# Kernel optimization log

Measured on AMD Instinct MI355X. Metric: run time of the kernel, lower is better.

## Reference

```python
import jax, jax.numpy as jnp
import numpy as np
from jax import lax

K, N = 256, 65536

def setup_inputs() -> dict:
    key = jax.random.key(0)
    k1, k2, k3 = jax.random.split(key, 3)
    # obs: non-negative event counts [K, N]
    obs = jax.random.uniform(k1, (K, N), dtype=jnp.float32) * 4.0
    # Beta ~ U(1, 3) [K]
    Beta = 1.0 + 2.0 * jax.random.uniform(k2, (K,), dtype=jnp.float32)
    # Alpha ~ U(0, 0.01) [K, K]
    Alpha = 0.01 * jax.random.uniform(k3, (K, K), dtype=jnp.float32)
    return {"obs": obs, "Beta": Beta, "Alpha": Alpha}

def reference(obs, Beta, Alpha):
    # obs: [K, N], Beta: [K], Alpha: [K, K]
    Kk, Nn = obs.shape
    Mu0 = obs.mean(axis=1) / 10.0 + 0.01            # [K] background rate
    decay = jnp.exp(-Beta)                          # [K]

    # Exponential kernel sum S[t] = sum_{tp<t} obs[:,tp] * Beta * exp(-(t-tp)*Beta)
    # admits recursion H[t] = exp(-Beta) * (H[t-1] + obs[:, t-1]), S[t] = Beta * H[t]
    def step(h, o_prev):
        h_new = decay * (h + o_prev)
        return h_new, h_new

    _, H = lax.scan(step, jnp.zeros((Kk,), obs.dtype), obs[:, :Nn - 1].T)  # [N-1, K]
    S = H * Beta                                    # [N-1, K]
    # lam1[:, t] = softplus(Alpha @ S[t]) for t >= 1; lam1[:, 0] = 0 (by original code)
    lam = jax.nn.softplus(jnp.einsum('jk,tk->tj', Alpha, S))  # [N-1, K]
    lams1 = jnp.concatenate([jnp.zeros((Kk, 1), obs.dtype), lam.T], axis=1)  # [K, N]
    lams0 = jnp.broadcast_to(Mu0[:, None], (Kk, Nn))          # [K, N]

    Nloglams = obs * jnp.log(lams0 + lams1 + 1e-5)
    loglik = (Nloglams - lams0 - lams1).sum()
    return loglik, lams0, lams1
```

## Files before the change

### kernel.cpp

```cpp
#include <hip/hip_runtime.h>
#include <math.h>

#define KK 256
#define NN 65536
#define TT 128
#define WW 16
#define TPAD 264
#define NB (NN / TT)
#define NCHUNK (NB * 2)

typedef __bf16 bf16x8 __attribute__((ext_vector_type(8)));
typedef float f32x4 __attribute__((ext_vector_type(4)));

__global__ __launch_bounds__(256) void alpha_kernel(const float* __restrict__ Alpha,
                                                    __bf16* __restrict__ AlphaB,
                                                    float* __restrict__ out) {
  const int i = blockIdx.x * 256 + threadIdx.x;
  AlphaB[i] = (__bf16)Alpha[i];
  if (i == 0) out[0] = 0.f;
}

__global__ __launch_bounds__(512, 4) void main_kernel(const float* __restrict__ obs,
                                                      const float* __restrict__ Beta,
                                                      const __bf16* __restrict__ AlphaB,
                                                      float* __restrict__ out,
                                                      float* __restrict__ P) {
  __shared__ __bf16 Slds[TT][TPAD];
  const int tid = threadIdx.x;
  const int bid = blockIdx.x;
  const int tb = ((bid & 7) << 6) | (bid >> 3);
  const int t0 = tb * TT;

  {
    const int k = tid & 255;
    const int c = tid >> 8;
    const int tbase = t0 + (c << 6);
    const float beta = Beta[k];
    const float decay = expf(-beta);
    const float* row = obs + (size_t)k * NN;
    float g = 0.f;
    if (tbase > 0) {
      const float4* p = (const float4*)(row + tbase - WW);
#pragma unroll
      for (int i = 0; i < WW / 4; ++i) {
        float4 v = p[i];
        g = decay * (g + v.x);
        g = decay * (g + v.y);
        g = decay * (g + v.z);
        g = decay * (g + v.w);
      }
    }
    const int r0 = c << 6;
    Slds[r0][k] = (__bf16)(beta * g);
    const float4* q = (const float4*)(row + tbase);
    float s = 0.f;
#pragma unroll
    for (int i = 0; i < 15; ++i) {
      float4 v = q[i];
      s += (v.x + v.y) + (v.z + v.w);
      g = decay * (g + v.x); Slds[r0 + 4 * i + 1][k] = (__bf16)(beta * g);
      g = decay * (g + v.y); Slds[r0 + 4 * i + 2][k] = (__bf16)(beta * g);
      g = decay * (g + v.z); Slds[r0 + 4 * i + 3][k] = (__bf16)(beta * g);
      g = decay * (g + v.w); Slds[r0 + 4 * i + 4][k] = (__bf16)(beta * g);
    }
    {
      float4 v = q[15];
      s += (v.x + v.y) + (v.z + v.w);
      g = decay * (g + v.x); Slds[r0 + 61][k] = (__bf16)(beta * g);
      g = decay * (g + v.y); Slds[r0 + 62][k] = (__bf16)(beta * g);
      g = decay * (g + v.z); Slds[r0 + 63][k] = (__bf16)(beta * g);
    }
    P[(size_t)(2 * bid + c) * KK + k] = s;
  }
  __syncthreads();

  const int wave = tid >> 6;
  const int wj = wave & 3, wc = wave >> 2;
  const int lane = tid & 63;
  const int lquad = lane >> 4;
  const int l16 = lane & 15;

  f32x4 acc[4][4];
#pragma unroll
  for (int a = 0; a < 4; ++a)
#pragma unroll
    for (int b = 0; b < 4; ++b) acc[a][b] = (f32x4){0.f, 0.f, 0.f, 0.f};

  const __bf16* Abase = AlphaB + (size_t)(wj * 64 + l16) * KK + lquad * 8;
  for (int k0 = 0; k0 < KK; k0 += 32) {
    bf16x8 afrag[4], bfrag[4];
#pragma unroll
    for (int js = 0; js < 4; ++js)
      afrag[js] = *(const bf16x8*)(Abase + (size_t)js * 16 * KK + k0);
#pragma unroll
    for (int ts = 0; ts < 4; ++ts)
      bfrag[ts] = *(const bf16x8*)&Slds[wc * 64 + ts * 16 + l16][k0 + lquad * 8];
#pragma unroll
    for (int js = 0; js < 4; ++js)
#pragma unroll
      for (int ts = 0; ts < 4; ++ts)
        acc[js][ts] = __builtin_amdgcn_mfma_f32_16x16x32_bf16(
            afrag[js], bfrag[ts], acc[js][ts], 0, 0, 0);
  }

  float* lams1 = out + 1 + (size_t)KK * NN;
  const int tcol = t0 + wc * 64;
#pragma unroll
  for (int js = 0; js < 4; ++js) {
#pragma unroll
    for (int r = 0; r < 4; ++r) {
      const int j = wj * 64 + js * 16 + lquad * 4 + r;
      const size_t rowoff = (size_t)j * NN + tcol + l16;
#pragma unroll
      for (int ts = 0; ts < 4; ++ts) {
        float v = acc[js][ts][r];
        float lam = v + __logf(1.f + __expf(-v));
        if (tcol + ts * 16 + l16 == 0) lam = 0.f;
        lams1[rowoff + ts * 16] = lam;
      }
    }
  }
}

__global__ __launch_bounds__(512) void loglik_kernel(const float* __restrict__ obs,
                                                     const float* __restrict__ P,
                                                     float* __restrict__ out) {
  const int j = blockIdx.x;
  const int tid = threadIdx.x;

  float s = 0.f;
#pragma unroll
  for (int c = 0; c < NCHUNK / 512; ++c)
    s += P[(size_t)(tid + c * 512) * KK + j];
  __shared__ float red[512];
  red[tid] = s;
  __syncthreads();
  for (int off = 256; off > 0; off >>= 1) {
    if (tid < off) red[tid] += red[tid + off];
    __syncthreads();
  }
  const float m = red[0] * (1.0f / NN) * 0.1f + 0.01f;

  const float* orow = obs + (size_t)j * NN;
  float* l0row = out + 1 + (size_t)j * NN;
  float* l1row = l0row + (size_t)KK * NN;
  float partial = 0.f;
#pragma unroll 8
  for (int i = 0; i < NN / 512; ++i) {
    const int t = tid + i * 512;
    const float l1 = l1row[t];
    const float o = orow[t];
    l0row[t] = m;
    partial += o * __logf(m + l1 + 1e-5f) - m - l1;
  }

#pragma unroll
  for (int off = 32; off > 0; off >>= 1)
    partial += __shfl_down(partial, off, 64);
  __syncthreads();
  if ((tid & 63) == 0) red[tid >> 6] = partial;
  __syncthreads();
  if (tid == 0) {
    float t = 0.f;
#pragma unroll
    for (int w = 0; w < 8; ++w) t += red[w];
    atomicAdd(out, t);
  }
}

extern "C" void kernel_launch(void* const* d_in, const int* in_sizes, int n_in,
                              void* d_out, int out_size, void* d_ws, size_t ws_size,
                              hipStream_t stream) {
  const float* obs   = (const float*)d_in[0];
  const float* Beta  = (const float*)d_in[1];
  const float* Alpha = (const float*)d_in[2];
  float* out = (float*)d_out;

  __bf16* AlphaB = (__bf16*)d_ws;
  float* P = (float*)(AlphaB + (size_t)KK * KK);

  hipLaunchKernelGGL(alpha_kernel, dim3(KK), dim3(256), 0, stream, Alpha, AlphaB, out);
  hipLaunchKernelGGL(main_kernel, dim3(NB), dim3(512), 0, stream,
                     obs, Beta, AlphaB, out, P);
  hipLaunchKernelGGL(loglik_kernel, dim3(KK), dim3(512), 0, stream, obs, P, out);
}
```

Before: 232.8 us.

## Compute decay recurrence with 8-lane shuffle scan for coalesced obs reads

Replaces the per-thread sequential recurrence over one row (one thread per k, strided float4 loads across rows) with groups of 8 lanes that scan 8 consecutive time steps using a shuffle-based weighted prefix scan. Each group carries its state across 16 rounds, and the row sum is reduced with shuffles. This makes global reads of obs coalesced along time and removes the 16-sample warm-up approximation's dependence on per-thread float4 strides. Partial sums are now one per block, which simplifies the loglik reduction. The cost is extra shuffles and multiplies, plus the 16-step truncated history window is kept.

```diff
diff --git a/kernel.cpp b/kernel.cpp
--- a/kernel.cpp
+++ b/kernel.cpp
@@ -4,10 +4,8 @@
 #define KK 256
 #define NN 65536
 #define TT 128
-#define WW 16
 #define TPAD 264
 #define NB (NN / TT)
-#define NCHUNK (NB * 2)
 
 typedef __bf16 bf16x8 __attribute__((ext_vector_type(8)));
 typedef float f32x4 __attribute__((ext_vector_type(4)));
@@ -32,45 +30,52 @@
   const int t0 = tb * TT;
 
   {
-    const int k = tid & 255;
-    const int c = tid >> 8;
-    const int tbase = t0 + (c << 6);
-    const float beta = Beta[k];
-    const float decay = expf(-beta);
-    const float* row = obs + (size_t)k * NN;
-    float g = 0.f;
-    if (tbase > 0) {
-      const float4* p = (const float4*)(row + tbase - WW);
+    const int ell = tid & 7;
+    const int krow0 = tid >> 3;
+    for (int it = 0; it < 4; ++it) {
+      const int k = it * 64 + krow0;
+      const float beta = Beta[k];
+      const float d = expf(-beta);
+      const float d2 = d * d, d4 = d2 * d2, d8 = d4 * d4;
+      float dl = 1.f;
+      if (ell & 1) dl *= d;
+      if (ell & 2) dl *= d2;
+      if (ell & 4) dl *= d4;
+      const float* row = obs + (size_t)k * NN;
+      float Hc = 0.f;
+      if (t0 > 0) {
 #pragma unroll
-      for (int i = 0; i < WW / 4; ++i) {
-        float4 v = p[i];
-        g = decay * (g + v.x);
-        g = decay * (g + v.y);
-        g = decay * (g + v.z);
-        g = decay * (g + v.w);
+        for (int rnd = 0; rnd < 2; ++rnd) {
+          const float u = row[t0 - 16 + rnd * 8 + ell];
+          float X = u, y;
+          y = __shfl_up(X, 1, 8); X += (ell >= 1 ? d  * y : 0.f);
+          y = __shfl_up(X, 2, 8); X += (ell >= 2 ? d2 * y : 0.f);
+          y = __shfl_up(X, 4, 8); X += (ell >= 4 ? d4 * y : 0.f);
+          const float I7 = __shfl(X, 7, 8);
+          Hc = d8 * Hc + d * I7;
+        }
       }
+      float rsum = 0.f;
+#pragma unroll
+      for (int rnd = 0; rnd < 16; ++rnd) {
+        const int base = 8 * rnd;
+        const float u = row[t0 + base + ell];
+        rsum += u;
+        float X = u, y;
+        y = __shfl_up(X, 1, 8); X += (ell >= 1 ? d  * y : 0.f);
+        y = __shfl_up(X, 2, 8); X += (ell >= 2 ? d2 * y : 0.f);
+        y = __shfl_up(X, 4, 8); X += (ell >= 4 ? d4 * y : 0.f);
+        const float Ip = __shfl_up(X, 1, 8);
+        const float H = dl * Hc + (ell >= 1 ? d * Ip : 0.f);
+        Slds[base + ell][k] = (__bf16)(beta * H);
+        const float I7 = __shfl(X, 7, 8);
+        Hc = d8 * Hc + d * I7;
+      }
+      rsum += __shfl_down(rsum, 1, 8);
+      rsum += __shfl_down(rsum, 2, 8);
+      rsum += __shfl_down(rsum, 4, 8);
+      if (ell == 0) P[(size_t)tb * KK + k] = rsum;
     }
-    const int r0 = c << 6;
-    Slds[r0][k] = (__bf16)(beta * g);
-    const float4* q = (const float4*)(row + tbase);
-    float s = 0.f;
-#pragma unroll
-    for (int i = 0; i < 15; ++i) {
-      float4 v = q[i];
-      s += (v.x + v.y) + (v.z + v.w);
-      g = decay * (g + v.x); Slds[r0 + 4 * i + 1][k] = (__bf16)(beta * g);
-      g = decay * (g + v.y); Slds[r0 + 4 * i + 2][k] = (__bf16)(beta * g);
-      g = decay * (g + v.z); Slds[r0 + 4 * i + 3][k] = (__bf16)(beta * g);
-      g = decay * (g + v.w); Slds[r0 + 4 * i + 4][k] = (__bf16)(beta * g);
-    }
-    {
-      float4 v = q[15];
-      s += (v.x + v.y) + (v.z + v.w);
-      g = decay * (g + v.x); Slds[r0 + 61][k] = (__bf16)(beta * g);
-      g = decay * (g + v.y); Slds[r0 + 62][k] = (__bf16)(beta * g);
-      g = decay * (g + v.z); Slds[r0 + 63][k] = (__bf16)(beta * g);
-    }
-    P[(size_t)(2 * bid + c) * KK + k] = s;
   }
   __syncthreads();
 
@@ -128,10 +133,7 @@
   const int j = blockIdx.x;
   const int tid = threadIdx.x;
 
-  float s = 0.f;
-#pragma unroll
-  for (int c = 0; c < NCHUNK / 512; ++c)
-    s += P[(size_t)(tid + c * 512) * KK + j];
+  float s = P[(size_t)tid * KK + j];
   __shared__ float red[512];
   red[tid] = s;
   __syncthreads();
```

After: 228.5 us. About the same (-1.8%).
